# Kernel optimization log

Hardware: AMD Instinct MI355X
Metric: run time of the kernel (lower is better)

Reference implementation:

```python
import jax, jax.numpy as jnp
import numpy as np

EMBED = 2048
HEADS = 16
GROUPS = 4
HEAD_DIM = EMBED // HEADS  # 128
REPEATS = HEADS // GROUPS  # 4


def setup_inputs() -> dict:
    key = jax.random.key(0)
    ks = jax.random.split(key, 9)
    s = 1.0 / np.sqrt(EMBED)
    kv_dim = GROUPS * HEAD_DIM
    return {
        "x": jax.random.normal(ks[0], (2, 2048, EMBED), dtype=jnp.float32),
        "Wq": jax.random.normal(ks[1], (EMBED, EMBED), dtype=jnp.float32) * s,
        "bq": jnp.zeros((EMBED,), dtype=jnp.float32),
        "Wk": jax.random.normal(ks[2], (EMBED, kv_dim), dtype=jnp.float32) * s,
        "bk": jnp.zeros((kv_dim,), dtype=jnp.float32),
        "Wv": jax.random.normal(ks[3], (EMBED, kv_dim), dtype=jnp.float32) * s,
        "bv": jnp.zeros((kv_dim,), dtype=jnp.float32),
        "Wo": jax.random.normal(ks[4], (EMBED, EMBED), dtype=jnp.float32) * s,
        "bo": jnp.zeros((EMBED,), dtype=jnp.float32),
    }


def reference(x, Wq, bq, Wk, bk, Wv, bv, Wo, bo):
    b, t, e = x.shape
    q = x @ Wq + bq                                   # [b,t,e]
    k = x @ Wk + bk                                   # [b,t,g*d]
    v = x @ Wv + bv
    # [b, g, r, t, d] for q; [b, g, t, d] for k,v (repeat_interleave == group-major)
    q = q.reshape(b, t, GROUPS, REPEATS, HEAD_DIM).transpose(0, 2, 3, 1, 4)
    k = k.reshape(b, t, GROUPS, HEAD_DIM).transpose(0, 2, 1, 3)
    v = v.reshape(b, t, GROUPS, HEAD_DIM).transpose(0, 2, 1, 3)
    scale = 1.0 / np.sqrt(HEAD_DIM)
    scores = jnp.einsum('bgrqd,bgkd->bgrqk', q, k) * scale
    causal = jnp.tril(jnp.ones((t, t), dtype=bool))
    scores = jnp.where(causal, scores, -jnp.inf)
    w = jax.nn.softmax(scores, axis=-1)
    out = jnp.einsum('bgrqk,bgkd->bgrqd', w, v)       # [b,g,r,t,d]
    out = out.transpose(0, 3, 1, 2, 4).reshape(b, t, e)
    return out @ Wo + bo
```

## Files before the change

### kernel.cpp

```cpp
#include <hip/hip_runtime.h>
#include <cstdint>

typedef __bf16 bf16;
typedef __attribute__((ext_vector_type(8))) __bf16 bf16x8;
typedef __attribute__((ext_vector_type(4))) __bf16 bf16x4;
typedef __attribute__((ext_vector_type(4))) float f32x4;
typedef __attribute__((ext_vector_type(4))) short short4_t;

__device__ __forceinline__ void load_lds16(const void* g, void* l) {
  __builtin_amdgcn_global_load_lds(
      (const __attribute__((address_space(1))) unsigned int*)g,
      (__attribute__((address_space(3))) unsigned int*)l, 16, 0, 0);
}

__device__ __forceinline__ float fast_exp2(float x) {
  float r;
  asm volatile("v_exp_f32 %0, %1" : "=v"(r) : "v"(x));
  return r;
}

template <bool OUT_F32, bool VSPLIT>
__global__ __launch_bounds__(256) void gemm_bt(
    const bf16* __restrict__ A, const bf16* __restrict__ Bt,
    const float* __restrict__ bias, void* __restrict__ Cv,
    int M, int N, int K, bf16* __restrict__ Vt) {
  __shared__ __align__(16) bf16 smem[VSPLIT ? 128 * 136 : 128 * 128];
  bf16* sA = smem;
  bf16* sB = smem + 128 * 64;
  const int t = threadIdx.x;
  const int w = t >> 6, lane = t & 63;
  const int quad = lane >> 4, l16 = lane & 15;
  const int wm = (w >> 1) * 64, wn = (w & 1) * 64;
  const int bm = blockIdx.y * 128, bn = blockIdx.x * 128;

  f32x4 acc[4][4] = {};
  const int srow = lane >> 3;
  const int sg = lane & 7;

  for (int kt = 0; kt < (K >> 6); ++kt) {
    const int k0 = kt << 6;
#pragma unroll
    for (int c2 = 0; c2 < 4; ++c2) {
      int c = c2 * 4 + w;
      int row = c * 8 + srow;
      int gg = sg ^ (row & 7);
      load_lds16(A + (int64_t)(bm + row) * K + k0 + gg * 8, sA + c * 512);
      load_lds16(Bt + (int64_t)(bn + row) * K + k0 + gg * 8, sB + c * 512);
    }
    asm volatile("s_waitcnt vmcnt(0)" ::: "memory");
    __syncthreads();
#pragma unroll
    for (int ks = 0; ks < 2; ++ks) {
      bf16x8 af[4], bfr[4];
#pragma unroll
      for (int i = 0; i < 4; ++i) {
        int m = wm + i * 16 + l16;
        af[i] = *(const bf16x8*)(sA + m * 64 + (((ks * 4 + quad) ^ (l16 & 7)) * 8));
        int n = wn + i * 16 + l16;
        bfr[i] = *(const bf16x8*)(sB + n * 64 + (((ks * 4 + quad) ^ (l16 & 7)) * 8));
      }
#pragma unroll
      for (int i = 0; i < 4; ++i)
#pragma unroll
        for (int j = 0; j < 4; ++j)
          acc[i][j] = __builtin_amdgcn_mfma_f32_16x16x32_bf16(af[i], bfr[j],
                                                              acc[i][j], 0, 0, 0);
    }
    __syncthreads();
  }

  if (VSPLIT && bn >= 2560) {
#pragma unroll
    for (int i = 0; i < 4; ++i) {
      int m0 = wm + i * 16 + quad * 4;
#pragma unroll
      for (int j = 0; j < 4; ++j) {
        int n_l = wn + j * 16 + l16;
        float bvv = bias ? bias[bn + n_l] : 0.0f;
        bf16x4 o4;
#pragma unroll
        for (int r = 0; r < 4; ++r) o4[r] = (bf16)(acc[i][j][r] + bvv);
        *(bf16x4*)(smem + n_l * 136 + m0) = o4;
      }
    }
    __syncthreads();
    const int n_l = t >> 1, half = t & 1;
    const int g = (bn - 2560) >> 7;
    const int b2 = bm >> 11;
    const int t0 = (bm & 2047) + half * 64;
    bf16* dst = Vt + ((int64_t)((b2 * 4 + g) * 128 + n_l)) * 2048 + t0;
    const bf16* src = smem + n_l * 136 + half * 64;
#pragma unroll
    for (int c = 0; c < 8; ++c)
      *(bf16x8*)(dst + c * 8) = *(const bf16x8*)(src + c * 8);
    return;
  }

#pragma unroll
  for (int i = 0; i < 4; ++i) {
    int gm = bm + wm + i * 16 + quad * 4;
#pragma unroll
    for (int j = 0; j < 4; ++j) {
      int gn = bn + wn + j * 16 + l16;
      float bvv = bias ? bias[gn] : 0.0f;
#pragma unroll
      for (int r = 0; r < 4; ++r) {
        float v = acc[i][j][r] + bvv;
        if (OUT_F32)
          ((float*)Cv)[(int64_t)(gm + r) * N + gn] = v;
        else
          ((bf16*)Cv)[(int64_t)(gm + r) * N + gn] = (bf16)v;
      }
    }
  }
}

__global__ __launch_bounds__(256, 2) void attn(
    const bf16* __restrict__ QKV, const bf16* __restrict__ Vt,
    bf16* __restrict__ Out) {
  constexpr float CC = 0.08838834764831845f * 1.44269504088896f;
  __shared__ __align__(16) bf16 sK[2][64 * 128];
  __shared__ __align__(16) bf16 sV[2][128 * 64];

  const int t = threadIdx.x;
  const int w = t >> 6, lane = t & 63;
  const int quad = lane >> 4, l16 = lane & 15;
  const int h = blockIdx.y, b = blockIdx.z;
  const int p = (b == 0) ? (int)blockIdx.x : 15 - (int)blockIdx.x;
  const int g = h >> 2;
  const int wr0 = w * 16;
  const int kbase = 2048 + g * 128;
  const bf16* vtb = Vt + (int64_t)((b * 4 + g) * 128) * 2048;
  const int rk = lane >> 4, rv = lane >> 3, sgv = lane & 7;
  const int qrow0A = p * 64, qrow0B = (31 - p) * 64;
  const int niters = 32 - p;

  auto stage = [&](int n0, bf16* sKb, bf16* sVb) {
#pragma unroll
    for (int c2 = 0; c2 < 4; ++c2) {
      int c = c2 * 4 + w;
      int rowk = c * 4 + rk;
      int ggk = (l16 & 8) | ((l16 ^ rowk) & 7);
      load_lds16(QKV + (int64_t)(b * 2048 + n0 + rowk) * 3072 + kbase + ggk * 8,
                 sKb + c * 512);
      int rowv = c * 8 + rv;
      int ggv = sgv ^ (rowv & 7);
      load_lds16(vtb + (int64_t)rowv * 2048 + n0 + ggv * 8, sVb + c * 512);
    }
  };

  stage(0, sK[0], sV[0]);

  bf16x8 qreg[2][4];
#pragma unroll
  for (int u = 0; u < 2; ++u) {
    int qr = (u == 0 ? qrow0A : qrow0B);
#pragma unroll
    for (int ks = 0; ks < 4; ++ks) {
      bf16x8 v = *(const bf16x8*)(QKV +
          (int64_t)(b * 2048 + qr + wr0 + l16) * 3072 + h * 128 + ks * 32 +
          quad * 8);
#pragma unroll
      for (int e = 0; e < 8; ++e) v[e] = (bf16)((float)v[e] * CC);
      qreg[u][ks] = v;
    }
  }

  f32x4 oacc[2][8] = {};
  float mrow[2] = {-3.0e38f, -3.0e38f};
  float lrow[2] = {0.f, 0.f};

  for (int it = 0; it < niters; ++it) {
    const int cur = it & 1;
    const int n0 = it * 64;
    bf16* sKc = sK[cur];
    bf16* sVc = sV[cur];
    const bool actA = (it <= p);

    asm volatile("s_waitcnt vmcnt(0)\n\ts_barrier" ::: "memory");
    if (it + 1 < niters) stage(n0 + 64, sK[cur ^ 1], sV[cur ^ 1]);

    f32x4 sacc[2][4] = {};
    if (actA) {
#pragma unroll
      for (int ks = 0; ks < 4; ++ks) {
        bf16x8 ak[4];
#pragma unroll
        for (int mj = 0; mj < 4; ++mj) {
          int kvr = mj * 16 + l16;
          int G = ks * 4 + quad;
          int slot = (G & 8) | ((G ^ kvr) & 7);
          ak[mj] = *(const bf16x8*)(sKc + kvr * 128 + slot * 8);
        }
        __builtin_amdgcn_s_setprio(1);
#pragma unroll
        for (int mj = 0; mj < 4; ++mj) {
          sacc[0][mj] = __builtin_amdgcn_mfma_f32_16x16x32_bf16(
              ak[mj], qreg[0][ks], sacc[0][mj], 0, 0, 0);
          sacc[1][mj] = __builtin_amdgcn_mfma_f32_16x16x32_bf16(
              ak[mj], qreg[1][ks], sacc[1][mj], 0, 0, 0);
        }
        __builtin_amdgcn_s_setprio(0);
      }
    } else {
#pragma unroll
      for (int ks = 0; ks < 4; ++ks) {
        bf16x8 ak[4];
#pragma unroll
        for (int mj = 0; mj < 4; ++mj) {
          int kvr = mj * 16 + l16;
          int G = ks * 4 + quad;
          int slot = (G & 8) | ((G ^ kvr) & 7);
          ak[mj] = *(const bf16x8*)(sKc + kvr * 128 + slot * 8);
        }
        __builtin_amdgcn_s_setprio(1);
#pragma unroll
        for (int mj = 0; mj < 4; ++mj)
          sacc[1][mj] = __builtin_amdgcn_mfma_f32_16x16x32_bf16(
              ak[mj], qreg[1][ks], sacc[1][mj], 0, 0, 0);
        __builtin_amdgcn_s_setprio(0);
      }
    }

    short4_t pb[2][4];
    auto softmax_u = [&](int u, bool last, int qrow0u) {
      if (last) {
        int qg = qrow0u + wr0 + l16;
#pragma unroll
        for (int mj = 0; mj < 4; ++mj)
#pragma unroll
          for (int r = 0; r < 4; ++r) {
            int kv = n0 + mj * 16 + quad * 4 + r;
            if (kv > qg) sacc[u][mj][r] = -3.0e38f;
          }
      }
      f32x4 m01, m23;
#pragma unroll
      for (int r = 0; r < 4; ++r) {
        m01[r] = fmaxf(sacc[u][0][r], sacc[u][1][r]);
        m23[r] = fmaxf(sacc[u][2][r], sacc[u][3][r]);
      }
      float mx = fmaxf(fmaxf(fmaxf(m01[0], m01[1]), fmaxf(m01[2], m01[3])),
                       fmaxf(fmaxf(m23[0], m23[1]), fmaxf(m23[2], m23[3])));
      mx = fmaxf(mx, __shfl_xor(mx, 16));
      mx = fmaxf(mx, __shfl_xor(mx, 32));
      if (!__all(mx <= mrow[u] + 11.0f)) {
        float mnew = fmaxf(mrow[u], mx);
        float alpha = fast_exp2(mrow[u] - mnew);
        lrow[u] *= alpha;
#pragma unroll
        for (int dj = 0; dj < 8; ++dj)
#pragma unroll
          for (int r = 0; r < 4; ++r) oacc[u][dj][r] *= alpha;
        mrow[u] = mnew;
      }
      float rs = 0.f;
#pragma unroll
      for (int mj = 0; mj < 4; ++mj) {
        bf16x4 p4;
#pragma unroll
        for (int r = 0; r < 4; ++r) {
          float pv = fast_exp2(sacc[u][mj][r] - mrow[u]);
          rs += pv;
          p4[r] = (bf16)pv;
        }
        pb[u][mj] = __builtin_bit_cast(short4_t, p4);
      }
      rs += __shfl_xor(rs, 16);
      rs += __shfl_xor(rs, 32);
      lrow[u] += rs;
    };
    if (actA) softmax_u(0, it == p, qrow0A);
    softmax_u(1, it == niters - 1, qrow0B);

#pragma unroll
    for (int mj = 0; mj < 4; ++mj) {
      const int sbase = mj * 2 + (quad >> 1);
      const int soff = (quad & 1) * 4;
      short4_t av[8];
#pragma unroll
      for (int dj = 0; dj < 8; ++dj) {
        int d = dj * 16 + l16;
        av[dj] = *(const short4_t*)(sVc + d * 64 + ((sbase ^ (d & 7)) * 8) + soff);
      }
      __builtin_amdgcn_s_setprio(1);
      if (actA) {
#pragma unroll
        for (int dj = 0; dj < 8; ++dj) {
          oacc[0][dj] = __builtin_amdgcn_mfma_f32_16x16x16bf16_1k(
              av[dj], pb[0][mj], oacc[0][dj], 0, 0, 0);
          oacc[1][dj] = __builtin_amdgcn_mfma_f32_16x16x16bf16_1k(
              av[dj], pb[1][mj], oacc[1][dj], 0, 0, 0);
        }
      } else {
#pragma unroll
        for (int dj = 0; dj < 8; ++dj)
          oacc[1][dj] = __builtin_amdgcn_mfma_f32_16x16x16bf16_1k(
              av[dj], pb[1][mj], oacc[1][dj], 0, 0, 0);
      }
      __builtin_amdgcn_s_setprio(0);
    }
  }

#pragma unroll
  for (int u = 0; u < 2; ++u) {
    int qrow0u = (u == 0 ? qrow0A : qrow0B);
    float inv = 1.0f / lrow[u];
    int64_t grow = b * 2048 + qrow0u + wr0 + l16;
#pragma unroll
    for (int dj = 0; dj < 8; ++dj) {
      bf16x4 o4;
#pragma unroll
      for (int r = 0; r < 4; ++r) o4[r] = (bf16)(oacc[u][dj][r] * inv);
      *(bf16x4*)(Out + grow * 2048 + h * 128 + dj * 16 + quad * 4) = o4;
    }
  }
}

__device__ __forceinline__ void tr_tile(const float* __restrict__ W,
                                        bf16* __restrict__ Wt, int K, int N,
                                        int bx, int by, int t, float* tile) {
  int tx = t & 63, ty = t >> 6;
#pragma unroll
  for (int q2 = 0; q2 < 16; ++q2) {
    int r = ty + q2 * 4;
    tile[r * 65 + tx] = W[(int64_t)(by * 64 + r) * N + bx * 64 + tx];
  }
  __syncthreads();
#pragma unroll
  for (int q2 = 0; q2 < 16; ++q2) {
    int n = ty + q2 * 4;
    Wt[(int64_t)(bx * 64 + n) * K + by * 64 + tx] = (bf16)tile[tx * 65 + n];
  }
}

__global__ __launch_bounds__(256) void prep(
    const float* __restrict__ x, const float* __restrict__ Wq,
    const float* __restrict__ Wk, const float* __restrict__ Wv,
    const float* __restrict__ Wo, const float* __restrict__ bq,
    const float* __restrict__ bk, const float* __restrict__ bv,
    bf16* __restrict__ xb, bf16* __restrict__ wqkvT, bf16* __restrict__ woT,
    float* __restrict__ bqkv) {
  __shared__ float tile[64 * 65];
  const int bid = blockIdx.x;
  const int t = threadIdx.x;
  if (bid < 8192) {
    int idx = bid * 256 + t;
    float4 v = ((const float4*)x)[idx];
    bf16x4 o = {(bf16)v.x, (bf16)v.y, (bf16)v.z, (bf16)v.w};
    ((bf16x4*)xb)[idx] = o;
  } else if (bid < 8192 + 1024) {
    int b2 = bid - 8192;
    tr_tile(Wq, wqkvT, 2048, 2048, b2 & 31, b2 >> 5, t, tile);
  } else if (bid < 8192 + 1024 + 256) {
    int b2 = bid - (8192 + 1024);
    tr_tile(Wk, wqkvT + 2048 * 2048, 2048, 512, b2 & 7, b2 >> 3, t, tile);
  } else if (bid < 8192 + 1024 + 512) {
    int b2 = bid - (8192 + 1024 + 256);
    tr_tile(Wv, wqkvT + 2560 * 2048, 2048, 512, b2 & 7, b2 >> 3, t, tile);
  } else if (bid < 8192 + 1024 + 512 + 1024) {
    int b2 = bid - (8192 + 1024 + 512);
    tr_tile(Wo, woT, 2048, 2048, b2 & 31, b2 >> 5, t, tile);
  } else {
    int i = (bid - (8192 + 1024 + 512 + 1024)) * 256 + t;
    if (i < 3072)
      bqkv[i] = i < 2048 ? bq[i] : (i < 2560 ? bk[i - 2048] : bv[i - 2560]);
  }
}

extern "C" void kernel_launch(void* const* d_in, const int* in_sizes, int n_in,
                              void* d_out, int out_size, void* d_ws,
                              size_t ws_size, hipStream_t stream) {
  const float* x = (const float*)d_in[0];
  const float* Wq = (const float*)d_in[1];
  const float* bq = (const float*)d_in[2];
  const float* Wk = (const float*)d_in[3];
  const float* bk = (const float*)d_in[4];
  const float* Wv = (const float*)d_in[5];
  const float* bv = (const float*)d_in[6];
  const float* Wo = (const float*)d_in[7];
  const float* bo = (const float*)d_in[8];
  float* out = (float*)d_out;

  char* ws = (char*)d_ws;
  bf16* xb = (bf16*)(ws);
  bf16* wqkvT = (bf16*)(ws + 16777216);
  bf16* woT = (bf16*)(ws + 29360128);
  float* bqkv = (float*)(ws + 37748736);
  bf16* qkv = (bf16*)(ws + 37761024);
  bf16* vt = (bf16*)(ws + 62926848);
  bf16* attnb = (bf16*)(ws + 67121152);

  prep<<<8192 + 1024 + 512 + 1024 + 12, 256, 0, stream>>>(
      x, Wq, Wk, Wv, Wo, bq, bk, bv, xb, wqkvT, woT, bqkv);

  gemm_bt<false, true><<<dim3(24, 32), 256, 0, stream>>>(
      xb, wqkvT, bqkv, qkv, 4096, 3072, 2048, vt);
  attn<<<dim3(16, 16, 2), 256, 0, stream>>>(qkv, vt, attnb);
  gemm_bt<true, false><<<dim3(16, 32), 256, 0, stream>>>(
      attnb, woT, bo, out, 4096, 2048, 2048, nullptr);
}
```

Measured before the change: 297.7 us.

## Add 256x256 double-buffered 8-wave GEMM for QKV projection

Replaces the 128x128 single-buffered QKV projection GEMM with a 256x256 tile, 512-thread kernel that double-buffers LDS. It splits each K-step into four phases that interleave global-to-LDS prefetch of the next tile with MFMA work, using explicit waitcnt, barriers and setprio. It also remaps workgroup IDs for better L2 locality. The intent is to hide global load latency and raise data reuse per tile. The risk is only 192 workgroups on a large GPU, plus high register and LDS pressure.

```diff
diff --git a/kernel.cpp b/kernel.cpp
--- a/kernel.cpp
+++ b/kernel.cpp
@@ -19,14 +19,220 @@
   return r;
 }
 
+#define BAR() asm volatile("s_barrier" ::: "memory")
+#define LGKM0()                                         \
+  do {                                                  \
+    asm volatile("s_waitcnt lgkmcnt(0)" ::: "memory");  \
+    __builtin_amdgcn_sched_barrier(0);                  \
+  } while (0)
+
 template <bool OUT_F32, bool VSPLIT>
+__global__ __launch_bounds__(512, 2) void gemm_bt256(
+    const bf16* __restrict__ A, const bf16* __restrict__ Bt,
+    const float* __restrict__ bias, void* __restrict__ Cv,
+    int M, int N, int K, bf16* __restrict__ Vt) {
+  __shared__ __align__(16) bf16 smem[VSPLIT ? 67584 : 65536];
+  const int t = threadIdx.x;
+  const int w = t >> 6, lane = t & 63;
+  const int quad = lane >> 4, l16 = lane & 15;
+  const int wm = (w >> 2) * 128, wn = (w & 3) * 64;
+  const int nbx = gridDim.x;
+  const int nwg = nbx * gridDim.y;
+  const int orig = blockIdx.y * nbx + blockIdx.x;
+  const int id = (orig & 7) * (nwg >> 3) + (orig >> 3);
+  const int bm = (id / nbx) * 256, bn = (id % nbx) * 256;
+
+  const int rsw = lane >> 3;
+  const int gg = (lane & 7) ^ rsw;
+
+  auto stage = [&](const bf16* __restrict__ G, int grow0, int k0v, bf16* ldsb,
+                   int c) {
+    load_lds16(G + (int64_t)(grow0 + c * 64 + w * 8 + rsw) * K + k0v + gg * 8,
+               ldsb + (c * 64 + w * 8) * 64);
+  };
+
+  f32x4 acc[8][4] = {};
+  bf16x8 bfr[4][2];
+  const int NT = K >> 6;
+
+  bf16* const sA0 = smem;
+  bf16* const sB0 = smem + 32768;
+
+  {
+    stage(Bt, bn, 0, sB0, 0);
+    stage(Bt, bn, 0, sB0, 1);
+    stage(Bt, bn, 0, sB0, 2);
+    stage(Bt, bn, 0, sB0, 3);
+    stage(A, bm, 0, sA0, 0);
+    stage(A, bm, 0, sA0, 2);
+    stage(A, bm, 0, sA0, 1);
+    stage(A, bm, 0, sA0, 3);
+    asm volatile("s_waitcnt vmcnt(2)" ::: "memory");
+    BAR();
+  }
+
+  int cur = 0;
+  for (int kt = 0; kt < NT; ++kt) {
+    const int kn = (kt << 6) + 64;
+    bf16* const sAc = sA0 + cur * 16384;
+    bf16* const sBc = sB0 + cur * 16384;
+    bf16* const sAn = sA0 + (cur ^ 1) * 16384;
+    bf16* const sBn = sB0 + (cur ^ 1) * 16384;
+    const bool more = (kt + 1 < NT);
+
+    bf16x8 af[2][2];
+    auto ldA = [&](int ibase) {
+#pragma unroll
+      for (int i2 = 0; i2 < 2; ++i2)
+#pragma unroll
+        for (int ks = 0; ks < 2; ++ks)
+          af[i2][ks] = *(const bf16x8*)(sAc + (wm + (ibase + i2) * 16 + l16) * 64 +
+                                        (((ks * 4 + quad) ^ (l16 & 7)) * 8));
+    };
+
+#pragma unroll
+    for (int j = 0; j < 4; ++j)
+#pragma unroll
+      for (int ks = 0; ks < 2; ++ks)
+        bfr[j][ks] = *(const bf16x8*)(sBc + (wn + j * 16 + l16) * 64 +
+                                      (((ks * 4 + quad) ^ (l16 & 7)) * 8));
+    ldA(0);
+    if (more) {
+      stage(Bt, bn, kn, sBn, 0);
+      stage(Bt, bn, kn, sBn, 1);
+    }
+    BAR();
+    LGKM0();
+    __builtin_amdgcn_s_setprio(1);
+#pragma unroll
+    for (int ks = 0; ks < 2; ++ks)
+#pragma unroll
+      for (int i2 = 0; i2 < 2; ++i2)
+#pragma unroll
+        for (int j = 0; j < 4; ++j)
+          acc[i2][j] = __builtin_amdgcn_mfma_f32_16x16x32_bf16(
+              af[i2][ks], bfr[j][ks], acc[i2][j], 0, 0, 0);
+    __builtin_amdgcn_s_setprio(0);
+    BAR();
+
+    ldA(2);
+    if (more) {
+      stage(Bt, bn, kn, sBn, 2);
+      stage(Bt, bn, kn, sBn, 3);
+      asm volatile("s_waitcnt vmcnt(4)" ::: "memory");
+    } else {
+      asm volatile("s_waitcnt vmcnt(0)" ::: "memory");
+    }
+    BAR();
+    LGKM0();
+    __builtin_amdgcn_s_setprio(1);
+#pragma unroll
+    for (int ks = 0; ks < 2; ++ks)
+#pragma unroll
+      for (int i2 = 0; i2 < 2; ++i2)
+#pragma unroll
+        for (int j = 0; j < 4; ++j)
+          acc[2 + i2][j] = __builtin_amdgcn_mfma_f32_16x16x32_bf16(
+              af[i2][ks], bfr[j][ks], acc[2 + i2][j], 0, 0, 0);
+    __builtin_amdgcn_s_setprio(0);
+    BAR();
+
+    ldA(4);
+    if (more) {
+      stage(A, bm, kn, sAn, 0);
+      stage(A, bm, kn, sAn, 2);
+    }
+    BAR();
+    LGKM0();
+    __builtin_amdgcn_s_setprio(1);
+#pragma unroll
+    for (int ks = 0; ks < 2; ++ks)
+#pragma unroll
+      for (int i2 = 0; i2 < 2; ++i2)
+#pragma unroll
+        for (int j = 0; j < 4; ++j)
+          acc[4 + i2][j] = __builtin_amdgcn_mfma_f32_16x16x32_bf16(
+              af[i2][ks], bfr[j][ks], acc[4 + i2][j], 0, 0, 0);
+    __builtin_amdgcn_s_setprio(0);
+    BAR();
+
+    ldA(6);
+    if (more) {
+      stage(A, bm, kn, sAn, 1);
+      stage(A, bm, kn, sAn, 3);
+      asm volatile("s_waitcnt vmcnt(2)" ::: "memory");
+    }
+    BAR();
+    LGKM0();
+    __builtin_amdgcn_s_setprio(1);
+#pragma unroll
+    for (int ks = 0; ks < 2; ++ks)
+#pragma unroll
+      for (int i2 = 0; i2 < 2; ++i2)
+#pragma unroll
+        for (int j = 0; j < 4; ++j)
+          acc[6 + i2][j] = __builtin_amdgcn_mfma_f32_16x16x32_bf16(
+              af[i2][ks], bfr[j][ks], acc[6 + i2][j], 0, 0, 0);
+    __builtin_amdgcn_s_setprio(0);
+    BAR();
+
+    cur ^= 1;
+  }
+
+  if (VSPLIT && bn >= 2560) {
+#pragma unroll
+    for (int i = 0; i < 8; ++i) {
+      int m0 = wm + i * 16 + quad * 4;
+#pragma unroll
+      for (int j = 0; j < 4; ++j) {
+        int n_l = wn + j * 16 + l16;
+        float bvv = bias ? bias[bn + n_l] : 0.0f;
+        bf16x4 o4;
+#pragma unroll
+        for (int r = 0; r < 4; ++r) o4[r] = (bf16)(acc[i][j][r] + bvv);
+        *(bf16x4*)(smem + n_l * 264 + m0) = o4;
+      }
+    }
+    __syncthreads();
+    const int n_l = t >> 1, half = t & 1;
+    const int gcol = bn + n_l - 2560;
+    const int g = gcol >> 7, d = gcol & 127;
+    const int b2 = bm >> 11;
+    const int t0 = (bm & 2047) + half * 128;
+    bf16* dst = Vt + ((int64_t)((b2 * 4 + g) * 128 + d)) * 2048 + t0;
+    const bf16* src = smem + n_l * 264 + half * 128;
+#pragma unroll
+    for (int cc = 0; cc < 16; ++cc)
+      *(bf16x8*)(dst + cc * 8) = *(const bf16x8*)(src + cc * 8);
+    return;
+  }
+
+#pragma unroll
+  for (int i = 0; i < 8; ++i) {
+    int gm = bm + wm + i * 16 + quad * 4;
+#pragma unroll
+    for (int j = 0; j < 4; ++j) {
+      int gn = bn + wn + j * 16 + l16;
+      float bvv = bias ? bias[gn] : 0.0f;
+#pragma unroll
+      for (int r = 0; r < 4; ++r) {
+        float v = acc[i][j][r] + bvv;
+        if (OUT_F32)
+          ((float*)Cv)[(int64_t)(gm + r) * N + gn] = v;
+        else
+          ((bf16*)Cv)[(int64_t)(gm + r) * N + gn] = (bf16)v;
+      }
+    }
+  }
+}
+
+template <bool OUT_F32>
 __global__ __launch_bounds__(256) void gemm_bt(
     const bf16* __restrict__ A, const bf16* __restrict__ Bt,
     const float* __restrict__ bias, void* __restrict__ Cv,
-    int M, int N, int K, bf16* __restrict__ Vt) {
-  __shared__ __align__(16) bf16 smem[VSPLIT ? 128 * 136 : 128 * 128];
-  bf16* sA = smem;
-  bf16* sB = smem + 128 * 64;
+    int M, int N, int K) {
+  __shared__ __align__(16) bf16 sA[128 * 64];
+  __shared__ __align__(16) bf16 sB[128 * 64];
   const int t = threadIdx.x;
   const int w = t >> 6, lane = t & 63;
   const int quad = lane >> 4, l16 = lane & 15;
@@ -68,34 +274,6 @@
     }
     __syncthreads();
   }
-
-  if (VSPLIT && bn >= 2560) {
-#pragma unroll
-    for (int i = 0; i < 4; ++i) {
-      int m0 = wm + i * 16 + quad * 4;
-#pragma unroll
-      for (int j = 0; j < 4; ++j) {
-        int n_l = wn + j * 16 + l16;
-        float bvv = bias ? bias[bn + n_l] : 0.0f;
-        bf16x4 o4;
-#pragma unroll
-        for (int r = 0; r < 4; ++r) o4[r] = (bf16)(acc[i][j][r] + bvv);
-        *(bf16x4*)(smem + n_l * 136 + m0) = o4;
-      }
-    }
-    __syncthreads();
-    const int n_l = t >> 1, half = t & 1;
-    const int g = (bn - 2560) >> 7;
-    const int b2 = bm >> 11;
-    const int t0 = (bm & 2047) + half * 64;
-    bf16* dst = Vt + ((int64_t)((b2 * 4 + g) * 128 + n_l)) * 2048 + t0;
-    const bf16* src = smem + n_l * 136 + half * 64;
-#pragma unroll
-    for (int c = 0; c < 8; ++c)
-      *(bf16x8*)(dst + c * 8) = *(const bf16x8*)(src + c * 8);
-    return;
-  }
-
 #pragma unroll
   for (int i = 0; i < 4; ++i) {
     int gm = bm + wm + i * 16 + quad * 4;
@@ -394,9 +572,9 @@
   prep<<<8192 + 1024 + 512 + 1024 + 12, 256, 0, stream>>>(
       x, Wq, Wk, Wv, Wo, bq, bk, bv, xb, wqkvT, woT, bqkv);
 
-  gemm_bt<false, true><<<dim3(24, 32), 256, 0, stream>>>(
+  gemm_bt256<false, true><<<dim3(12, 16), 512, 0, stream>>>(
       xb, wqkvT, bqkv, qkv, 4096, 3072, 2048, vt);
   attn<<<dim3(16, 16, 2), 256, 0, stream>>>(qkv, vt, attnb);
-  gemm_bt<true, false><<<dim3(16, 32), 256, 0, stream>>>(
-      attnb, woT, bo, out, 4096, 2048, 2048, nullptr);
-}
+  gemm_bt<true><<<dim3(16, 32), 256, 0, stream>>>(attnb, woT, bo, out, 4096,
+                                                  2048, 2048);
+}
```

Result: slower. 306.8 us (+3.0%).

## Replace GEMM with double-buffered 256-row tiles, 512 threads, and XCD-aware block remap

Applied to the files above, without the earlier changes.

Both projection GEMMs move to a new kernel that uses 256xBN tiles with 8 waves. LDS is double-buffered so the next K-tile's global-to-LDS loads overlap the current MFMAs, with partial vmcnt waits and raw barriers. Work-group IDs are remapped across the 8 XCDs, and s_setprio is raised around the MFMA bursts. The larger tiles cut redundant global loads but use more registers and LDS and launch fewer blocks, which may lower occupancy and leave part of the wave underfilled.

```diff
diff --git a/kernel.cpp b/kernel.cpp
--- a/kernel.cpp
+++ b/kernel.cpp
@@ -19,88 +19,135 @@
   return r;
 }
 
-template <bool OUT_F32, bool VSPLIT>
-__global__ __launch_bounds__(256) void gemm_bt(
+#define BAR() asm volatile("s_barrier" ::: "memory")
+
+template <bool OUT_F32, bool VSPLIT, int BN>
+__global__ __launch_bounds__(512, 2) void gemm_dp(
     const bf16* __restrict__ A, const bf16* __restrict__ Bt,
     const float* __restrict__ bias, void* __restrict__ Cv,
     int M, int N, int K, bf16* __restrict__ Vt) {
-  __shared__ __align__(16) bf16 smem[VSPLIT ? 128 * 136 : 128 * 128];
-  bf16* sA = smem;
-  bf16* sB = smem + 128 * 64;
+  constexpr int BELEMS = BN * 64;
+  constexpr int NJ = BN / 64;
+  constexpr int NBS = BN / 64;
+  constexpr int SMEM = VSPLIT ? 67584 : (32768 + 2 * BELEMS);
+  __shared__ __align__(16) bf16 smem[SMEM];
   const int t = threadIdx.x;
   const int w = t >> 6, lane = t & 63;
   const int quad = lane >> 4, l16 = lane & 15;
-  const int wm = (w >> 1) * 64, wn = (w & 1) * 64;
-  const int bm = blockIdx.y * 128, bn = blockIdx.x * 128;
-
-  f32x4 acc[4][4] = {};
-  const int srow = lane >> 3;
-  const int sg = lane & 7;
-
-  for (int kt = 0; kt < (K >> 6); ++kt) {
-    const int k0 = kt << 6;
-#pragma unroll
-    for (int c2 = 0; c2 < 4; ++c2) {
-      int c = c2 * 4 + w;
-      int row = c * 8 + srow;
-      int gg = sg ^ (row & 7);
-      load_lds16(A + (int64_t)(bm + row) * K + k0 + gg * 8, sA + c * 512);
-      load_lds16(Bt + (int64_t)(bn + row) * K + k0 + gg * 8, sB + c * 512);
-    }
-    asm volatile("s_waitcnt vmcnt(0)" ::: "memory");
-    __syncthreads();
-#pragma unroll
-    for (int ks = 0; ks < 2; ++ks) {
-      bf16x8 af[4], bfr[4];
-#pragma unroll
-      for (int i = 0; i < 4; ++i) {
-        int m = wm + i * 16 + l16;
-        af[i] = *(const bf16x8*)(sA + m * 64 + (((ks * 4 + quad) ^ (l16 & 7)) * 8));
-        int n = wn + i * 16 + l16;
-        bfr[i] = *(const bf16x8*)(sB + n * 64 + (((ks * 4 + quad) ^ (l16 & 7)) * 8));
-      }
-#pragma unroll
-      for (int i = 0; i < 4; ++i)
-#pragma unroll
-        for (int j = 0; j < 4; ++j)
-          acc[i][j] = __builtin_amdgcn_mfma_f32_16x16x32_bf16(af[i], bfr[j],
-                                                              acc[i][j], 0, 0, 0);
-    }
-    __syncthreads();
+  const int wm = (w >> 2) * 128, wn = (w & 3) * (BN / 4);
+  const int nbx = gridDim.x;
+  const int nwg = nbx * gridDim.y;
+  const int orig = blockIdx.y * nbx + blockIdx.x;
+  const int id = (orig & 7) * (nwg >> 3) + (orig >> 3);
+  const int bm = (id / nbx) * 256, bn = (id % nbx) * BN;
+
+  const int rsw = lane >> 3;
+  const int gg = (lane & 7) ^ rsw;
+
+  auto stage = [&](const bf16* __restrict__ G, int grow0, int k0v, bf16* ldsb,
+                   int c) {
+    load_lds16(G + (int64_t)(grow0 + c * 64 + w * 8 + rsw) * K + k0v + gg * 8,
+               ldsb + (c * 64 + w * 8) * 64);
+  };
+
+  f32x4 acc[8][NJ] = {};
+  const int NT = K >> 6;
+
+  bf16* const sA0 = smem;
+  bf16* const sB0 = smem + 32768;
+
+#pragma unroll
+  for (int c = 0; c < 4; ++c) stage(A, bm, 0, sA0, c);
+#pragma unroll
+  for (int c = 0; c < NBS; ++c) stage(Bt, bn, 0, sB0, c);
+
+  int cur = 0;
+  for (int kt = 0; kt < NT; ++kt) {
+    const int kn = (kt << 6) + 64;
+    bf16* const sAc = sA0 + cur * 16384;
+    bf16* const sBc = sB0 + cur * BELEMS;
+
+    if (kt + 1 < NT) {
+      bf16* const sAn = sA0 + (cur ^ 1) * 16384;
+      bf16* const sBn = sB0 + (cur ^ 1) * BELEMS;
+#pragma unroll
+      for (int c = 0; c < 4; ++c) stage(A, bm, kn, sAn, c);
+#pragma unroll
+      for (int c = 0; c < NBS; ++c) stage(Bt, bn, kn, sBn, c);
+      if constexpr (NBS == 4)
+        asm volatile("s_waitcnt vmcnt(8)" ::: "memory");
+      else
+        asm volatile("s_waitcnt vmcnt(6)" ::: "memory");
+    } else {
+      asm volatile("s_waitcnt vmcnt(0)" ::: "memory");
+    }
+    BAR();
+
+    bf16x8 bfr[NJ][2];
+#pragma unroll
+    for (int j = 0; j < NJ; ++j)
+#pragma unroll
+      for (int ks = 0; ks < 2; ++ks)
+        bfr[j][ks] = *(const bf16x8*)(sBc + (wn + j * 16 + l16) * 64 +
+                                      (((ks * 4 + quad) ^ (l16 & 7)) * 8));
+#pragma unroll
+    for (int qd = 0; qd < 4; ++qd) {
+      bf16x8 af[2][2];
+#pragma unroll
+      for (int i2 = 0; i2 < 2; ++i2)
+#pragma unroll
+        for (int ks = 0; ks < 2; ++ks)
+          af[i2][ks] =
+              *(const bf16x8*)(sAc + (wm + (qd * 2 + i2) * 16 + l16) * 64 +
+                               (((ks * 4 + quad) ^ (l16 & 7)) * 8));
+      __builtin_amdgcn_s_setprio(1);
+#pragma unroll
+      for (int ks = 0; ks < 2; ++ks)
+#pragma unroll
+        for (int i2 = 0; i2 < 2; ++i2)
+#pragma unroll
+          for (int j = 0; j < NJ; ++j)
+            acc[qd * 2 + i2][j] = __builtin_amdgcn_mfma_f32_16x16x32_bf16(
+                af[i2][ks], bfr[j][ks], acc[qd * 2 + i2][j], 0, 0, 0);
+      __builtin_amdgcn_s_setprio(0);
+    }
+    BAR();
+    cur ^= 1;
   }
 
   if (VSPLIT && bn >= 2560) {
 #pragma unroll
-    for (int i = 0; i < 4; ++i) {
+    for (int i = 0; i < 8; ++i) {
       int m0 = wm + i * 16 + quad * 4;
 #pragma unroll
-      for (int j = 0; j < 4; ++j) {
+      for (int j = 0; j < NJ; ++j) {
         int n_l = wn + j * 16 + l16;
         float bvv = bias ? bias[bn + n_l] : 0.0f;
         bf16x4 o4;
 #pragma unroll
         for (int r = 0; r < 4; ++r) o4[r] = (bf16)(acc[i][j][r] + bvv);
-        *(bf16x4*)(smem + n_l * 136 + m0) = o4;
+        *(bf16x4*)(smem + n_l * 264 + m0) = o4;
       }
     }
     __syncthreads();
     const int n_l = t >> 1, half = t & 1;
-    const int g = (bn - 2560) >> 7;
+    const int gcol = bn + n_l - 2560;
+    const int g = gcol >> 7, d = gcol & 127;
     const int b2 = bm >> 11;
-    const int t0 = (bm & 2047) + half * 64;
-    bf16* dst = Vt + ((int64_t)((b2 * 4 + g) * 128 + n_l)) * 2048 + t0;
-    const bf16* src = smem + n_l * 136 + half * 64;
-#pragma unroll
-    for (int c = 0; c < 8; ++c)
-      *(bf16x8*)(dst + c * 8) = *(const bf16x8*)(src + c * 8);
+    const int t0 = (bm & 2047) + half * 128;
+    bf16* dst = Vt + ((int64_t)((b2 * 4 + g) * 128 + d)) * 2048 + t0;
+    const bf16* src = smem + n_l * 264 + half * 128;
+#pragma unroll
+    for (int cc = 0; cc < 16; ++cc)
+      *(bf16x8*)(dst + cc * 8) = *(const bf16x8*)(src + cc * 8);
     return;
   }
 
 #pragma unroll
-  for (int i = 0; i < 4; ++i) {
+  for (int i = 0; i < 8; ++i) {
     int gm = bm + wm + i * 16 + quad * 4;
 #pragma unroll
-    for (int j = 0; j < 4; ++j) {
+    for (int j = 0; j < NJ; ++j) {
       int gn = bn + wn + j * 16 + l16;
       float bvv = bias ? bias[gn] : 0.0f;
 #pragma unroll
@@ -394,9 +441,9 @@
   prep<<<8192 + 1024 + 512 + 1024 + 12, 256, 0, stream>>>(
       x, Wq, Wk, Wv, Wo, bq, bk, bv, xb, wqkvT, woT, bqkv);
 
-  gemm_bt<false, true><<<dim3(24, 32), 256, 0, stream>>>(
+  gemm_dp<false, true, 256><<<dim3(12, 16), 512, 0, stream>>>(
       xb, wqkvT, bqkv, qkv, 4096, 3072, 2048, vt);
   attn<<<dim3(16, 16, 2), 256, 0, stream>>>(qkv, vt, attnb);
-  gemm_bt<true, false><<<dim3(16, 32), 256, 0, stream>>>(
+  gemm_dp<true, false, 128><<<dim3(16, 16), 512, 0, stream>>>(
       attnb, woT, bo, out, 4096, 2048, 2048, nullptr);
 }
```

New measurement: 301.4 us. Within noise of the previous version (+1.2%).
